# Kernel optimization log

Measured on AMD Instinct MI355X. Metric: run time of the kernel, lower is better.

The kernel has to match this reference:

```python
import jax, jax.numpy as jnp
import numpy as np


def setup_inputs() -> dict:
    key = jax.random.key(0)
    k1, k2 = jax.random.split(key)
    p_hat = jax.random.normal(k1, (16384, 3), dtype=jnp.float32)
    p = jax.random.normal(k2, (16384, 3), dtype=jnp.float32)
    return {"p_hat": p_hat, "p": p}


def reference(p_hat, p):
    # squared pairwise L2 distances: ||a-b||^2 = ||a||^2 + ||b||^2 - 2 a.b
    a2 = jnp.sum(p_hat * p_hat, axis=-1)            # [N]
    b2 = jnp.sum(p * p, axis=-1)                    # [M]
    cross = p_hat @ p.T                             # [N, M]
    d2 = jnp.maximum(a2[:, None] + b2[None, :] - 2.0 * cross, 0.0)
    # Chamfer: mean of col-mins (min over dim 0) + mean of row-mins (min over dim 1)
    return jnp.mean(jnp.min(d2, axis=0)) + jnp.mean(jnp.min(d2, axis=1))
```

## Files before the change

kernel.cpp:

```cpp
#include <hip/hip_runtime.h>

#define N 16384
#define TPB 256
#define INF_BITS 0x7F800000

#define NT32 (N / 32)
#define MT 4
#define NSTRIP (NT32 / MT)
#define NJSPLIT 16
#define JW (NT32 / NJSPLIT)
#define NWAVES (2 * NSTRIP * NJSPLIT)
#define NBLK_MFMA (NWAVES / 4)
#define FRAG_U4 (NT32 * 64)
#define WS_NEED_MFMA (4ull * FRAG_U4 * sizeof(uint4) + 2ull * N * sizeof(int))

using bf16x8 = __attribute__((ext_vector_type(8))) short;
using fx16   = __attribute__((ext_vector_type(16))) float;

__device__ __forceinline__ unsigned short bf16_rn(float f) {
    unsigned u = __float_as_uint(f);
    u += 0x7FFFu + ((u >> 16) & 1u);
    return (unsigned short)(u >> 16);
}
__device__ __forceinline__ float bf16f(unsigned short h) {
    return __uint_as_float(((unsigned)h) << 16);
}
__device__ __forceinline__ uint4 pack8(const unsigned short* a) {
    return make_uint4((unsigned)a[0] | ((unsigned)a[1] << 16),
                      (unsigned)a[2] | ((unsigned)a[3] << 16),
                      (unsigned)a[4] | ((unsigned)a[5] << 16),
                      (unsigned)a[6] | ((unsigned)a[7] << 16));
}

__global__ void pack_mfma(const float* __restrict__ p_hat, const float* __restrict__ p,
                          uint4* __restrict__ frags, int* __restrict__ minbuf)
{
    int idx = blockIdx.x * blockDim.x + threadIdx.x;
    if (idx >= 2 * N) return;
    minbuf[idx] = INF_BITS;
    const float* src = (idx < N) ? p_hat : p;
    int i = (idx < N) ? idx : idx - N;
    float x = src[3*i+0], y = src[3*i+1], z = src[3*i+2];

    unsigned short xh = bf16_rn(x), yh = bf16_rn(y), zh = bf16_rn(z);
    unsigned short xl = bf16_rn(x - bf16f(xh));
    unsigned short yl = bf16_rn(y - bf16f(yh));
    unsigned short zl = bf16_rn(z - bf16f(zh));
    float s = __builtin_fmaf(x, x, __builtin_fmaf(y, y, z * z));
    unsigned short sh = bf16_rn(s), sl = bf16_rn(s - bf16f(sh));
    unsigned short m2xh = bf16_rn(-2.0f * bf16f(xh)), m2xl = bf16_rn(-2.0f * bf16f(xl));
    unsigned short m2yh = bf16_rn(-2.0f * bf16f(yh)), m2yl = bf16_rn(-2.0f * bf16f(yl));
    unsigned short m2zh = bf16_rn(-2.0f * bf16f(zh)), m2zl = bf16_rn(-2.0f * bf16f(zl));
    const unsigned short one = 0x3F80;

    unsigned short q[16] = { m2xh, m2xh, m2xl, m2xl, m2yh, m2yh, m2yl, m2yl,
                             m2zh, m2zh, m2zl, m2zl, sh, sl, one, one };
    unsigned short r[16] = { xh, xl, xh, xl, yh, yl, yh, yl,
                             zh, zl, zh, zl, one, one, sh, sl };

    uint4* Qa = frags + ((idx < N) ? 0 : FRAG_U4);
    uint4* Ra = frags + 2 * FRAG_U4 + ((idx < N) ? 0 : FRAG_U4);
    int t = i >> 5, rr = i & 31;
    Qa[t * 64 +      rr] = pack8(q);
    Qa[t * 64 + 32 + rr] = pack8(q + 8);
    Ra[t * 64 +      rr] = pack8(r);
    Ra[t * 64 + 32 + rr] = pack8(r + 8);
}

__global__ void __launch_bounds__(TPB, 2) chamfer_mfma(const uint4* __restrict__ frags,
                                                       int* __restrict__ minbuf)
{
    int lane = threadIdx.x & 63;
    int wid  = blockIdx.x * 4 + (int)(threadIdx.x >> 6);
    int strip  = wid & (NSTRIP - 1);
    int jsplit = (wid >> 7) & (NJSPLIT - 1);
    int pass   = wid >> 11;

    const uint4* Q = frags + (pass ? FRAG_U4 : 0);
    const uint4* R = frags + 2 * FRAG_U4 + (pass ? 0 : FRAG_U4);

    bf16x8 A[MT];
#pragma unroll
    for (int m = 0; m < MT; ++m)
        A[m] = __builtin_bit_cast(bf16x8, Q[(strip * MT + m) * 64 + lane]);

    fx16 zf;
#pragma unroll
    for (int r2 = 0; r2 < 16; ++r2) zf[r2] = 0.0f;
    fx16 rmin[MT];
#pragma unroll
    for (int m = 0; m < MT; ++m)
#pragma unroll
        for (int r2 = 0; r2 < 16; ++r2) rmin[m][r2] = __builtin_inff();

    const uint4* Rj = R + jsplit * (JW * 64) + lane;
    uint4 ca = Rj[0];
    uint4 cb = Rj[64];
    for (int jj = 0; jj < JW; jj += 2) {
        int n2 = (jj + 2 < JW) ? (jj + 2) : 0;
        int n3 = (jj + 2 < JW) ? (jj + 3) : 1;
        uint4 na = Rj[n2 * 64];
        uint4 nb = Rj[n3 * 64];
        bf16x8 Ba = __builtin_bit_cast(bf16x8, ca);
        bf16x8 Bb = __builtin_bit_cast(bf16x8, cb);
#pragma unroll
        for (int m = 0; m < MT; ++m) {
            fx16 da = __builtin_amdgcn_mfma_f32_32x32x16_bf16(A[m], Ba, zf, 0, 0, 0);
            fx16 db = __builtin_amdgcn_mfma_f32_32x32x16_bf16(A[m], Bb, zf, 0, 0, 0);
#pragma unroll
            for (int r2 = 0; r2 < 16; ++r2) {
                rmin[m][r2] = fminf(rmin[m][r2], fminf(da[r2], db[r2]));
            }
        }
        ca = na; cb = nb;
    }

    int rowbase = pass * N + strip * (MT * 32) + 4 * (lane >> 5);
#pragma unroll
    for (int m = 0; m < MT; ++m) {
#pragma unroll
        for (int r2 = 0; r2 < 16; ++r2) {
            float v = rmin[m][r2];
            v = fminf(v, __shfl_xor(v, 1));
            v = fminf(v, __shfl_xor(v, 2));
            v = fminf(v, __shfl_xor(v, 4));
            v = fminf(v, __shfl_xor(v, 8));
            v = fminf(v, __shfl_xor(v, 16));
            if ((lane & 31) == 0) {
                int row = rowbase + m * 32 + (r2 & 3) + 8 * (r2 >> 2);
                atomicMin(&minbuf[row], __float_as_int(fmaxf(v, 0.0f)));
            }
        }
    }
}

__global__ void __launch_bounds__(1024) reduce_kernel(const int* __restrict__ minbuf,
                                                      float* __restrict__ out) {
    const int4* mb4 = (const int4*)minbuf;
    float s = 0.0f;
#pragma unroll
    for (int k = 0; k < (2 * N / 4) / 1024; ++k) {
        int4 v = mb4[k * 1024 + threadIdx.x];
        s += __int_as_float(v.x) + __int_as_float(v.y) +
             __int_as_float(v.z) + __int_as_float(v.w);
    }
    for (int off = 32; off > 0; off >>= 1) s += __shfl_down(s, off, 64);
    __shared__ float partial[1024 / 64];
    int lane = threadIdx.x & 63;
    int wid  = threadIdx.x >> 6;
    if (lane == 0) partial[wid] = s;
    __syncthreads();
    if (threadIdx.x == 0) {
        float t = 0.0f;
        for (int w = 0; w < 1024 / 64; ++w) t += partial[w];
        out[0] = t / (float)N;
    }
}

#define OQPT 4
#define OQTILE (TPB * OQPT)
#define ONQT (N / OQTILE)
#define OSPLIT 64
#define OCHUNK (N / OSPLIT)
#define OGRID (2 * OSPLIT * ONQT)

__global__ void pack_old(const float* __restrict__ p_hat, const float* __restrict__ p,
                         float4* __restrict__ q4, int* __restrict__ minbuf) {
    int idx = blockIdx.x * blockDim.x + threadIdx.x;
    if (idx >= 2 * N) return;
    const float* src = (idx < N) ? p_hat : p;
    int k = (idx < N) ? idx : idx - N;
    float x = src[3*k+0], y = src[3*k+1], z = src[3*k+2];
    q4[idx] = make_float4(x, y, z, x*x + y*y + z*z);
    minbuf[idx] = INF_BITS;
}

__global__ void __launch_bounds__(TPB) chamfer_old(const float4* __restrict__ q4,
                                                   int* __restrict__ minbuf) {
    int b = blockIdx.x;
    int dir = b & 1;
    int rest = b >> 1;
    int jc = rest & (OSPLIT - 1);
    int qt = rest >> 6;
    const float4* __restrict__ qp = q4 + (dir ? N : 0);
    const float4* __restrict__ rp = q4 + (dir ? 0 : N);
    int ibase = qt * OQTILE + (int)threadIdx.x;
    float m2x[OQPT], m2y[OQPT], m2z[OQPT], qw[OQPT], vmin[OQPT];
#pragma unroll
    for (int q = 0; q < OQPT; ++q) {
        float4 qq = qp[ibase + q * TPB];
        m2x[q] = -2.0f * qq.x; m2y[q] = -2.0f * qq.y; m2z[q] = -2.0f * qq.z;
        qw[q] = qq.w; vmin[q] = __builtin_inff();
    }
    int j0 = jc * OCHUNK;
    float4 ra = rp[j0];
    float4 rb = rp[j0 + 1];
#pragma unroll 2
    for (int j = j0; j < j0 + OCHUNK; j += 2) {
        float4 na = rp[j + 2];
        float4 nb = rp[j + 3];
        float raw = ra.w, rbw = rb.w;
#pragma unroll
        for (int q = 0; q < OQPT; ++q) {
            float ta = __builtin_fmaf(ra.x, m2x[q],
                       __builtin_fmaf(ra.y, m2y[q],
                       __builtin_fmaf(ra.z, m2z[q], raw)));
            float tb = __builtin_fmaf(rb.x, m2x[q],
                       __builtin_fmaf(rb.y, m2y[q],
                       __builtin_fmaf(rb.z, m2z[q], rbw)));
            vmin[q] = fminf(vmin[q], fminf(ta, tb));
        }
        ra = na; rb = nb;
    }
#pragma unroll
    for (int q = 0; q < OQPT; ++q) {
        float m = fmaxf(vmin[q] + qw[q], 0.0f);
        atomicMin(&minbuf[dir * N + ibase + q * TPB], __float_as_int(m));
    }
}

extern "C" void kernel_launch(void* const* d_in, const int* in_sizes, int n_in,
                              void* d_out, int out_size, void* d_ws, size_t ws_size,
                              hipStream_t stream) {
    const float* p_hat = (const float*)d_in[0];
    const float* p     = (const float*)d_in[1];
    float* out = (float*)d_out;
    if (ws_size >= WS_NEED_MFMA) {
        uint4* frags = (uint4*)d_ws;
        int* minbuf  = (int*)((char*)d_ws + 4ull * FRAG_U4 * sizeof(uint4));
        pack_mfma<<<(2 * N + TPB - 1) / TPB, TPB, 0, stream>>>(p_hat, p, frags, minbuf);
        chamfer_mfma<<<NBLK_MFMA, TPB, 0, stream>>>(frags, minbuf);
        reduce_kernel<<<1, 1024, 0, stream>>>(minbuf, out);
    } else {
        float4* q4  = (float4*)d_ws;
        int* minbuf = (int*)((char*)d_ws + 2 * N * sizeof(float4));
        pack_old<<<(2 * N + TPB - 1) / TPB, TPB, 0, stream>>>(p_hat, p, q4, minbuf);
        chamfer_old<<<OGRID, TPB, 0, stream>>>(q4, minbuf);
        reduce_kernel<<<1, 1024, 0, stream>>>(minbuf, out);
    }
}
```

Measured before the change: 100.9 us.

## Compute row and column minima in a single pass over the distance matrix

Drops the second pass that recomputed the transposed distance matrix for column minima. Each wave now also reduces its MFMA tiles along rows, combines the two half-waves with a lane shuffle, and writes per-column minima with atomicMin. This halves the MFMA work and wave count, in exchange for extra min instructions, a shuffle and many global atomics inside the inner loop.

Measured after the change: 97.83 us. 1.03x faster.

```diff
diff --git a/kernel.cpp b/kernel.cpp
--- a/kernel.cpp
+++ b/kernel.cpp
@@ -9,7 +9,7 @@
 #define NSTRIP (NT32 / MT)
 #define NJSPLIT 16
 #define JW (NT32 / NJSPLIT)
-#define NWAVES (2 * NSTRIP * NJSPLIT)
+#define NWAVES (NSTRIP * NJSPLIT)
 #define NBLK_MFMA (NWAVES / 4)
 #define FRAG_U4 (NT32 * 64)
 #define WS_NEED_MFMA (4ull * FRAG_U4 * sizeof(uint4) + 2ull * N * sizeof(int))
@@ -30,6 +30,13 @@
                       (unsigned)a[2] | ((unsigned)a[3] << 16),
                       (unsigned)a[4] | ((unsigned)a[5] << 16),
                       (unsigned)a[6] | ((unsigned)a[7] << 16));
+}
+__device__ __forceinline__ float tree16(const fx16& d) {
+    float a = fminf(fminf(fminf(d[0], d[1]), fminf(d[2], d[3])),
+                    fminf(fminf(d[4], d[5]), fminf(d[6], d[7])));
+    float b = fminf(fminf(fminf(d[8], d[9]), fminf(d[10], d[11])),
+                    fminf(fminf(d[12], d[13]), fminf(d[14], d[15])));
+    return fminf(a, b);
 }
 
 __global__ void pack_mfma(const float* __restrict__ p_hat, const float* __restrict__ p,
@@ -73,11 +80,10 @@
     int lane = threadIdx.x & 63;
     int wid  = blockIdx.x * 4 + (int)(threadIdx.x >> 6);
     int strip  = wid & (NSTRIP - 1);
-    int jsplit = (wid >> 7) & (NJSPLIT - 1);
-    int pass   = wid >> 11;
-
-    const uint4* Q = frags + (pass ? FRAG_U4 : 0);
-    const uint4* R = frags + 2 * FRAG_U4 + (pass ? 0 : FRAG_U4);
+    int jsplit = wid >> 7;
+
+    const uint4* Q = frags;
+    const uint4* R = frags + 3 * FRAG_U4;
 
     bf16x8 A[MT];
 #pragma unroll
@@ -94,6 +100,7 @@
         for (int r2 = 0; r2 < 16; ++r2) rmin[m][r2] = __builtin_inff();
 
     const uint4* Rj = R + jsplit * (JW * 64) + lane;
+    int colbase = N + (jsplit * JW) * 32;
     uint4 ca = Rj[0];
     uint4 cb = Rj[64];
     for (int jj = 0; jj < JW; jj += 2) {
@@ -103,19 +110,29 @@
         uint4 nb = Rj[n3 * 64];
         bf16x8 Ba = __builtin_bit_cast(bf16x8, ca);
         bf16x8 Bb = __builtin_bit_cast(bf16x8, cb);
+        float cma = __builtin_inff();
+        float cmb = __builtin_inff();
 #pragma unroll
         for (int m = 0; m < MT; ++m) {
             fx16 da = __builtin_amdgcn_mfma_f32_32x32x16_bf16(A[m], Ba, zf, 0, 0, 0);
             fx16 db = __builtin_amdgcn_mfma_f32_32x32x16_bf16(A[m], Bb, zf, 0, 0, 0);
 #pragma unroll
-            for (int r2 = 0; r2 < 16; ++r2) {
+            for (int r2 = 0; r2 < 16; ++r2)
                 rmin[m][r2] = fminf(rmin[m][r2], fminf(da[r2], db[r2]));
-            }
+            cma = fminf(cma, tree16(da));
+            cmb = fminf(cmb, tree16(db));
+        }
+        cma = fminf(cma, __shfl_xor(cma, 32));
+        cmb = fminf(cmb, __shfl_xor(cmb, 32));
+        if (lane < 32) {
+            int c0 = colbase + jj * 32 + lane;
+            atomicMin(&minbuf[c0],      __float_as_int(fmaxf(cma, 0.0f)));
+            atomicMin(&minbuf[c0 + 32], __float_as_int(fmaxf(cmb, 0.0f)));
         }
         ca = na; cb = nb;
     }
 
-    int rowbase = pass * N + strip * (MT * 32) + 4 * (lane >> 5);
+    int rowbase = strip * (MT * 32) + 4 * (lane >> 5);
 #pragma unroll
     for (int m = 0; m < MT; ++m) {
 #pragma unroll
```
